# Kernel optimization log

Hardware: AMD Instinct MI355X
Metric: run time of the kernel (lower is better)

Reference implementation:

```python
import jax, jax.numpy as jnp
import numpy as np

N, E = 100000, 640000
H, EDGE_D, ATOM_D, RD, L = 128, 10, 25, 64, 4


def _gelu(t):
    return jax.nn.gelu(t, approximate=True)  # tanh approximation, matches torch GELU(approximate='tanh')


def _mlp2(t, w1, b1, w2, b2):
    return _gelu(t @ w1 + b1) @ w2 + b2


def setup_inputs() -> dict:
    key = jax.random.key(0)
    ks = iter(jax.random.split(key, 64))
    s = 0.05
    d = {}
    d['x'] = jax.random.normal(next(ks), (N, ATOM_D), jnp.float32)
    d['edge_index'] = jax.random.randint(next(ks), (2, E), 0, N, jnp.int32)
    d['edge_attr'] = jax.random.normal(next(ks), (E, EDGE_D), jnp.float32)
    d['enc_w1'] = jax.random.normal(next(ks), (ATOM_D, H)) * s
    d['enc_b1'] = jnp.zeros((H,))
    d['enc_w2'] = jax.random.normal(next(ks), (H, H)) * s
    d['enc_b2'] = jnp.zeros((H,))
    d['edge_w1'] = jax.random.normal(next(ks), (L, EDGE_D, H)) * s
    d['edge_b1'] = jnp.zeros((L, H))
    d['edge_w2'] = jax.random.normal(next(ks), (L, H, H)) * s
    d['edge_b2'] = jnp.zeros((L, H))
    d['msg_w1'] = jax.random.normal(next(ks), (L, H, H)) * s
    d['msg_b1'] = jnp.zeros((L, H))
    d['msg_w2'] = jax.random.normal(next(ks), (L, H, H)) * s
    d['msg_b2'] = jnp.zeros((L, H))
    d['gate_w'] = jax.random.normal(next(ks), (L, 2 * H, H)) * s
    d['gate_b'] = jnp.zeros((L, H))
    d['ln_g'] = jnp.ones((L, H))
    d['ln_b'] = jnp.zeros((L, H))
    for name in ('ion', 'pka', 'acid'):
        d[name + '_w1'] = jax.random.normal(next(ks), (H, RD)) * s
        d[name + '_b1'] = jnp.zeros((RD,))
        d[name + '_w2'] = jax.random.normal(next(ks), (RD, 1)) * s
        d[name + '_b2'] = jnp.zeros((1,))
    return d


def reference(x, edge_index, edge_attr, enc_w1, enc_b1, enc_w2, enc_b2,
              edge_w1, edge_b1, edge_w2, edge_b2,
              msg_w1, msg_b1, msg_w2, msg_b2,
              gate_w, gate_b, ln_g, ln_b,
              ion_w1, ion_b1, ion_w2, ion_b2,
              pka_w1, pka_b1, pka_w2, pka_b2,
              acid_w1, acid_b1, acid_w2, acid_b2):
    src, dst = edge_index[0], edge_index[1]
    n = x.shape[0]
    h = _mlp2(x, enc_w1, enc_b1, enc_w2, enc_b2)  # [N, H]
    ones_e = jnp.ones((src.shape[0],), x.dtype)
    count = jnp.clip(jax.ops.segment_sum(ones_e, dst, num_segments=n), 1.0)[:, None]  # [N,1]
    for i in range(L):
        ew = _mlp2(edge_attr, edge_w1[i], edge_b1[i], edge_w2[i], edge_b2[i])  # [E, H]
        msg = _mlp2(h[src], msg_w1[i], msg_b1[i], msg_w2[i], msg_b2[i]) * ew   # [E, H]
        agg = jax.ops.segment_sum(msg, dst, num_segments=n) / count           # [N, H] mean agg
        gate = jax.nn.sigmoid(jnp.concatenate([h, agg], axis=-1) @ gate_w[i] + gate_b[i])
        h = h + gate * agg
        mu = jnp.mean(h, axis=-1, keepdims=True)
        var = jnp.mean(jnp.square(h - mu), axis=-1, keepdims=True)
        h = (h - mu) * jax.lax.rsqrt(var + 1e-5) * ln_g[i] + ln_b[i]
    ion = _mlp2(h, ion_w1, ion_b1, ion_w2, ion_b2)
    pka = _mlp2(h, pka_w1, pka_b1, pka_w2, pka_b2)
    acid = _mlp2(h, acid_w1, acid_b1, acid_w2, acid_b2)
    return (ion, pka, acid)
```

## Files before the change

### kernel.cpp

```cpp
#include <hip/hip_runtime.h>
#include <math.h>

#define NN 100000
#define NN2 100032
#define NE 640000
#define H 128
#define AD 25
#define ED 10
#define RD 64
#define NL 4
#define NB_E (NE / 64 + 1)
#define NSB ((NN + 255) / 256)
#define CAP 256

typedef short bfrag __attribute__((ext_vector_type(8)));
typedef float floatx4 __attribute__((ext_vector_type(4)));
typedef unsigned short ushort;

#define MFMA(a, b, c) __builtin_amdgcn_mfma_f32_16x16x32_bf16(a, b, c, 0, 0, 0)

__device__ __forceinline__ ushort f2bf(float f) {
    unsigned u = __float_as_uint(f);
    unsigned r = (u + 0x7FFFu + ((u >> 16) & 1u)) >> 16;
    return (ushort)r;
}
__device__ __forceinline__ float bf2f(ushort b) {
    return __uint_as_float(((unsigned)b) << 16);
}
__device__ __forceinline__ float gelu_t(float x) {
    float u = 0.7978845608028654f * (x + 0.044715f * x * x * x);
    float e = __expf(2.0f * u);
    float th = 1.0f - 2.0f / (e + 1.0f);
    return 0.5f * x * (1.0f + th);
}
__device__ __forceinline__ float sigm(float x) {
    return 1.0f / (1.0f + __expf(-x));
}

__global__ void k_wtall(ushort* __restrict__ wt,
                        const float* __restrict__ s0, const float* __restrict__ s1,
                        const float* __restrict__ s2, const float* __restrict__ s3,
                        const float* __restrict__ s4, const float* __restrict__ s5,
                        const float* __restrict__ s6, const float* __restrict__ s7,
                        const float* __restrict__ s8, const float* __restrict__ s9) {
    int idx = blockIdx.x * 256 + threadIdx.x;
    const float* src;
    int Ks, N, Kd, off;
    if (idx < 4096)        { src = s0; Ks = 25;  N = 128; Kd = 32;  off = 0; }
    else if (idx < 20480)  { src = s1; Ks = 128; N = 128; Kd = 128; off = 4096; }
    else if (idx < 36864)  { src = s2; Ks = 10;  N = 128; Kd = 32;  off = 20480; }
    else if (idx < 102400) { src = s3; Ks = 128; N = 128; Kd = 128; off = 36864; }
    else if (idx < 167936) { src = s4; Ks = 128; N = 128; Kd = 128; off = 102400; }
    else if (idx < 233472) { src = s5; Ks = 128; N = 128; Kd = 128; off = 167936; }
    else if (idx < 364544) { src = s6; Ks = 256; N = 128; Kd = 256; off = 233472; }
    else if (idx < 372736) { src = s7; Ks = 128; N = 64;  Kd = 128; off = 364544; }
    else if (idx < 380928) { src = s8; Ks = 128; N = 64;  Kd = 128; off = 372736; }
    else if (idx < 389120) { src = s9; Ks = 128; N = 64;  Kd = 128; off = 380928; }
    else return;
    int lidx = idx - off;
    int nk = N * Kd;
    int b = lidx / nk;
    int rem = lidx - b * nk;
    int n = rem / Kd, k = rem - n * Kd;
    float v = (k < Ks) ? src[((size_t)b * Ks + k) * N + n] : 0.0f;
    wt[idx] = f2bf(v);
}

__global__ void k_cvt(const float* __restrict__ src, ushort* __restrict__ dst,
                      int rs, int Ks, int Kd, int total) {
    for (int idx = blockIdx.x * 256 + threadIdx.x; idx < total; idx += gridDim.x * 256) {
        int r = idx / Kd, k = idx - r * Kd;
        dst[idx] = (r < rs && k < Ks) ? f2bf(src[(size_t)r * Ks + k]) : 0;
    }
}
__global__ void k_cvtperm(const float* __restrict__ ea, const int* __restrict__ perm,
                          ushort* __restrict__ out) {
    int j = blockIdx.x * 256 + threadIdx.x;
    if (j >= NE) return;
    const float* src = ea + (size_t)perm[j] * ED;
    unsigned u[8];
#pragma unroll
    for (int k = 0; k < 5; ++k)
        u[k] = (unsigned)f2bf(src[2 * k]) | ((unsigned)f2bf(src[2 * k + 1]) << 16);
    u[5] = u[6] = u[7] = 0u;
    uint4* o = (uint4*)(out + (size_t)j * 16);
    uint4 a; a.x = u[0]; a.y = u[1]; a.z = u[2]; a.w = u[3];
    uint4 b; b.x = u[4]; b.y = u[5]; b.z = u[6]; b.w = u[7];
    o[0] = a; o[1] = b;
}

__global__ void k_hist(const int* __restrict__ ei, int* __restrict__ hist) {
    int e = blockIdx.x * 256 + threadIdx.x;
    if (e < NE) atomicAdd(&hist[ei[NE + e]], 1);
}
__global__ void k_scan1(const int* __restrict__ hist, int* __restrict__ incl,
                        int* __restrict__ bsum) {
    __shared__ int s[256];
    int tid = threadIdx.x;
    int i = blockIdx.x * 256 + tid;
    s[tid] = (i < NN) ? hist[i] : 0;
    __syncthreads();
    for (int off = 1; off < 256; off <<= 1) {
        int t = (tid >= off) ? s[tid - off] : 0;
        __syncthreads();
        s[tid] += t;
        __syncthreads();
    }
    if (i < NN) incl[i] = s[tid];
    if (tid == 255) bsum[blockIdx.x] = s[255];
}
__global__ void k_scan2(int* __restrict__ bsum) {
    __shared__ int s[512];
    int tid = threadIdx.x;
    s[tid] = (tid < NSB) ? bsum[tid] : 0;
    __syncthreads();
    for (int off = 1; off < 512; off <<= 1) {
        int t = (tid >= off) ? s[tid - off] : 0;
        __syncthreads();
        s[tid] += t;
        __syncthreads();
    }
    if (tid < NSB) bsum[tid] = (tid > 0) ? s[tid - 1] : 0;
}
__global__ void k_scan3(const int* __restrict__ hist, const int* __restrict__ incl,
                        const int* __restrict__ bsum, int* __restrict__ row_ptr) {
    int i = blockIdx.x * 256 + threadIdx.x;
    if (i < NN) row_ptr[i] = bsum[blockIdx.x] + incl[i] - hist[i];
    if (i == 0) row_ptr[NN] = NE;
}
__global__ void k_scatter(const int* __restrict__ ei, int* __restrict__ cursor,
                          int* __restrict__ perm) {
    int e = blockIdx.x * 256 + threadIdx.x;
    if (e < NE) {
        int d = ei[NE + e];
        int pos = atomicAdd(&cursor[d], 1);
        perm[pos] = e;
    }
}
__global__ void k_blockrange(const int* __restrict__ row_ptr, int* __restrict__ nf,
                             int* __restrict__ nl) {
    int n = blockIdx.x * 256 + threadIdx.x;
    if (n < NN) {
        int b = row_ptr[n] >> 6;
        atomicMin(&nf[b], n);
        atomicMax(&nl[b], n);
    }
}

template <int K1>
__global__ void __launch_bounds__(256)
k_mlp2mf(const ushort* __restrict__ Abf, ushort* __restrict__ Obf,
         const ushort* __restrict__ W1t, const float* __restrict__ B1,
         const ushort* __restrict__ W2t, const float* __restrict__ B2) {
    __shared__ ushort sH[64 * 136];
    const int tid = threadIdx.x;
    const int w = tid >> 6, lane = tid & 63, lr = lane & 15, lg = lane >> 4;
    const int rowB = blockIdx.x * 64 + w * 16 + lr;

    bfrag bvv[K1 / 32];
#pragma unroll
    for (int kb = 0; kb < K1 / 32; ++kb)
        bvv[kb] = *(const bfrag*)(Abf + (size_t)rowB * K1 + kb * 32 + lg * 8);

    floatx4 acc[8];
#pragma unroll
    for (int t = 0; t < 8; ++t) acc[t] = (floatx4){0.f, 0.f, 0.f, 0.f};
#pragma unroll
    for (int kb = 0; kb < K1 / 32; ++kb) {
#pragma unroll
        for (int t = 0; t < 8; ++t) {
            bfrag av = *(const bfrag*)(W1t + (t * 16 + lr) * K1 + kb * 32 + lg * 8);
            acc[t] = MFMA(av, bvv[kb], acc[t]);
        }
    }
    ushort* sHrow = sH + (w * 16 + lr) * 136;
#pragma unroll
    for (int t = 0; t < 8; ++t) {
        const float4 b1 = *(const float4*)(B1 + t * 16 + lg * 4);
        float h0 = gelu_t(acc[t][0] + b1.x), h1 = gelu_t(acc[t][1] + b1.y);
        float h2 = gelu_t(acc[t][2] + b1.z), h3 = gelu_t(acc[t][3] + b1.w);
        uint2 p;
        p.x = (unsigned)f2bf(h0) | ((unsigned)f2bf(h1) << 16);
        p.y = (unsigned)f2bf(h2) | ((unsigned)f2bf(h3) << 16);
        *(uint2*)(sHrow + t * 16 + lg * 4) = p;
    }
#pragma unroll
    for (int t = 0; t < 8; ++t) acc[t] = (floatx4){0.f, 0.f, 0.f, 0.f};
#pragma unroll
    for (int kb = 0; kb < 4; ++kb) {
        bfrag av = *(const bfrag*)(sH + (w * 16 + lr) * 136 + kb * 32 + lg * 8);
#pragma unroll
        for (int t = 0; t < 8; ++t) {
            bfrag bv = *(const bfrag*)(W2t + (t * 16 + lr) * 128 + kb * 32 + lg * 8);
            acc[t] = MFMA(av, bv, acc[t]);
        }
    }
    const int rowD = blockIdx.x * 64 + w * 16 + lg * 4;
#pragma unroll
    for (int t = 0; t < 8; ++t) {
        const int col = t * 16 + lr;
        const float b2 = B2[col];
#pragma unroll
        for (int r = 0; r < 4; ++r) {
            int row = rowD + r;
            if (row < NN) Obf[(size_t)row * 128 + col] = f2bf(acc[t][r] + b2);
        }
    }
}

__global__ void __launch_bounds__(256)
k_ew(const ushort* __restrict__ eap, ushort* __restrict__ ewp, int S,
     const ushort* __restrict__ W1t, const float* __restrict__ B1,
     const ushort* __restrict__ W2t, const float* __restrict__ B2) {
    __shared__ ushort sea[128 * 40];
    __shared__ ushort sH[4][16 * 136];
    const int tid = threadIdx.x;
    const int w = tid >> 6, lane = tid & 63, lr = lane & 15, lg = lane >> 4;
    const int jl0 = blockIdx.x * 128;

    {
        int r = tid >> 1, half = tid & 1;
        int j = S + jl0 + r;
        uint4 z; z.x = z.y = z.z = z.w = 0u;
        uint4 v = z;
        if (j < NE) v = *(const uint4*)(eap + (size_t)j * 16 + half * 8);
        *(uint4*)(sea + r * 40 + half * 8) = v;
        *(uint4*)(sea + r * 40 + 16 + half * 8) = z;
    }
    bfrag av1[8];
#pragma unroll
    for (int t = 0; t < 8; ++t)
        av1[t] = *(const bfrag*)(W1t + (t * 16 + lr) * 32 + lg * 8);
    __syncthreads();

    for (int rt = 0; rt < 2; ++rt) {
        const int row_l = w * 32 + rt * 16;
        floatx4 acc[8];
#pragma unroll
        for (int t = 0; t < 8; ++t) acc[t] = (floatx4){0.f, 0.f, 0.f, 0.f};
        bfrag bv = *(const bfrag*)(sea + (row_l + lr) * 40 + lg * 8);
#pragma unroll
        for (int t = 0; t < 8; ++t) acc[t] = MFMA(av1[t], bv, acc[t]);
        ushort* sHr = sH[w] + lr * 136;
#pragma unroll
        for (int t = 0; t < 8; ++t) {
            const float4 b1 = *(const float4*)(B1 + t * 16 + lg * 4);
            float h0 = gelu_t(acc[t][0] + b1.x), h1 = gelu_t(acc[t][1] + b1.y);
            float h2 = gelu_t(acc[t][2] + b1.z), h3 = gelu_t(acc[t][3] + b1.w);
            uint2 p;
            p.x = (unsigned)f2bf(h0) | ((unsigned)f2bf(h1) << 16);
            p.y = (unsigned)f2bf(h2) | ((unsigned)f2bf(h3) << 16);
            *(uint2*)(sHr + t * 16 + lg * 4) = p;
        }
#pragma unroll
        for (int t = 0; t < 8; ++t) acc[t] = (floatx4){0.f, 0.f, 0.f, 0.f};
#pragma unroll
        for (int kb = 0; kb < 4; ++kb) {
            bfrag av = *(const bfrag*)(sH[w] + lr * 136 + kb * 32 + lg * 8);
#pragma unroll
            for (int t = 0; t < 8; ++t) {
                bfrag bw = *(const bfrag*)(W2t + (t * 16 + lr) * 128 + kb * 32 + lg * 8);
                acc[t] = MFMA(bw, av, acc[t]);
            }
        }
        const int jl = jl0 + row_l + lr;
        if (S + jl < NE) {
            ushort* orow = ewp + (size_t)jl * 128;
#pragma unroll
            for (int t = 0; t < 8; ++t) {
                const float4 b2 = *(const float4*)(B2 + t * 16 + lg * 4);
                uint2 p;
                p.x = (unsigned)f2bf(acc[t][0] + b2.x) |
                      ((unsigned)f2bf(acc[t][1] + b2.y) << 16);
                p.y = (unsigned)f2bf(acc[t][2] + b2.z) |
                      ((unsigned)f2bf(acc[t][3] + b2.w) << 16);
                *(uint2*)(orow + t * 16 + lg * 4) = p;
            }
        }
    }
}

__global__ void __launch_bounds__(256)
k_gms(const int* __restrict__ ei, const int* __restrict__ perm,
      const int* __restrict__ row_ptr, const int* __restrict__ nf,
      const int* __restrict__ nl, const ushort* __restrict__ ewp, int S,
      const ushort* __restrict__ mbf, ushort* __restrict__ aggbf) {
    __shared__ int ssrc[CAP], sdst[CAP], sseg[CAP];
    __shared__ int snode[64];
    __shared__ float sinvd[64];
    __shared__ float sagg[64 * 132];
    __shared__ int swtot[4];
    __shared__ int s_nseg;

    const int b = blockIdx.x;
    const int n0 = nf[b];
    if (n0 >= NN) return;
    const int n1 = nl[b];
    const int e0 = row_ptr[n0];
    int ne = row_ptr[n1 + 1] - e0;
    if (ne <= 0) return;
    const int ncl = (ne < CAP) ? ne : CAP;

    const int tid = threadIdx.x;
    const int w = tid >> 6, lane = tid & 63;

    for (int i = tid; i < 64 * 132; i += 256) sagg[i] = 0.0f;

    int dstv = -1 - tid;
    if (tid < ncl) {
        int e = perm[e0 + tid];
        ssrc[tid] = ei[e];
        dstv = ei[NE + e];
    }
    sdst[tid] = dstv;
    __syncthreads();

    int f = 0;
    if (tid < ncl) f = (tid == 0) ? 1 : (sdst[tid] != sdst[tid - 1]);
    unsigned long long mk = __ballot(f);
    int incl = __popcll(mk & (~0ull >> (63 - lane)));
    if (lane == 63) swtot[w] = incl;
    __syncthreads();
    int woff = 0;
    for (int i = 0; i < w; ++i) woff += swtot[i];
    int segid = woff + incl;
    sseg[tid] = segid - 1;
    if (f) {
        int s = segid - 1;
        snode[s] = dstv;
        sinvd[s] = 1.0f / (float)(row_ptr[dstv + 1] - row_ptr[dstv]);
    }
    if (tid == 255) s_nseg = segid;
    __syncthreads();
    const int nseg = s_nseg;

    const int c0 = (tid & 31) * 4;
    const int g = tid >> 5;
    const int chunk = (ncl + 7) >> 3;
    const int j0 = g * chunk;
    const int j1 = (j0 + chunk < ncl) ? (j0 + chunk) : ncl;
    const int be = e0 - S;
    int cs = -1;
    float v0 = 0.f, v1 = 0.f, v2 = 0.f, v3 = 0.f;
    uint2 ewc, mvc;
    if (j0 < j1) {
        ewc = *(const uint2*)(ewp + (size_t)(be + j0) * 128 + c0);
        mvc = *(const uint2*)(mbf + (size_t)ssrc[j0] * 128 + c0);
    }
    for (int j = j0; j < j1; ++j) {
        uint2 ewn = ewc, mvn = mvc;
        if (j + 1 < j1) {
            ewn = *(const uint2*)(ewp + (size_t)(be + j + 1) * 128 + c0);
            mvn = *(const uint2*)(mbf + (size_t)ssrc[j + 1] * 128 + c0);
        }
        float a0 = bf2f((ushort)(ewc.x & 0xFFFF)) * bf2f((ushort)(mvc.x & 0xFFFF));
        float a1 = bf2f((ushort)(ewc.x >> 16)) * bf2f((ushort)(mvc.x >> 16));
        float a2 = bf2f((ushort)(ewc.y & 0xFFFF)) * bf2f((ushort)(mvc.y & 0xFFFF));
        float a3 = bf2f((ushort)(ewc.y >> 16)) * bf2f((ushort)(mvc.y >> 16));
        int sg = sseg[j];
        if (sg != cs) {
            if (cs >= 0) {
                float* p = &sagg[cs * 132 + c0];
                atomicAdd(p + 0, v0); atomicAdd(p + 1, v1);
                atomicAdd(p + 2, v2); atomicAdd(p + 3, v3);
            }
            cs = sg; v0 = a0; v1 = a1; v2 = a2; v3 = a3;
        } else {
            v0 += a0; v1 += a1; v2 += a2; v3 += a3;
        }
        ewc = ewn; mvc = mvn;
    }
    if (cs >= 0) {
        float* p = &sagg[cs * 132 + c0];
        atomicAdd(p + 0, v0); atomicAdd(p + 1, v1);
        atomicAdd(p + 2, v2); atomicAdd(p + 3, v3);
    }
    __syncthreads();
    for (int i = tid; i < nseg * 32; i += 256) {
        int s = i >> 5, qd = i & 31;
        float inv = sinvd[s];
        const float* p = &sagg[s * 132 + qd * 4];
        uint2 pk;
        pk.x = (unsigned)f2bf(p[0] * inv) | ((unsigned)f2bf(p[1] * inv) << 16);
        pk.y = (unsigned)f2bf(p[2] * inv) | ((unsigned)f2bf(p[3] * inv) << 16);
        *(uint2*)(aggbf + (size_t)snode[s] * 128 + qd * 4) = pk;
    }
}

template <int WITH_MSG>
__global__ void __launch_bounds__(256)
k_gatemlp(ushort* __restrict__ hbf, const ushort* __restrict__ aggbf,
          const ushort* __restrict__ GWt, const float* __restrict__ GB,
          const float* __restrict__ LNG, const float* __restrict__ LNB,
          const ushort* __restrict__ W1t, const float* __restrict__ B1,
          const ushort* __restrict__ W2t, const float* __restrict__ B2,
          ushort* __restrict__ mbf) {
    __shared__ ushort sA[64 * 136];
    const int tid = threadIdx.x;
    const int w = tid >> 6, lane = tid & 63, lr = lane & 15, lg = lane >> 4;
    const int row = blockIdx.x * 64 + w * 16 + lr;

    bfrag bvv[8];
    uint2 hp[8], ap[8];
#pragma unroll
    for (int kb = 0; kb < 4; ++kb)
        bvv[kb] = *(const bfrag*)(hbf + (size_t)row * 128 + kb * 32 + lg * 8);
#pragma unroll
    for (int kb = 0; kb < 4; ++kb)
        bvv[4 + kb] = *(const bfrag*)(aggbf + (size_t)row * 128 + kb * 32 + lg * 8);
#pragma unroll
    for (int t = 0; t < 8; ++t) {
        hp[t] = *(const uint2*)(hbf + (size_t)row * 128 + t * 16 + lg * 4);
        ap[t] = *(const uint2*)(aggbf + (size_t)row * 128 + t * 16 + lg * 4);
    }

    floatx4 acc[8];
#pragma unroll
    for (int t = 0; t < 8; ++t) acc[t] = (floatx4){0.f, 0.f, 0.f, 0.f};
#pragma unroll
    for (int kb = 0; kb < 8; ++kb) {
#pragma unroll
        for (int t = 0; t < 8; ++t) {
            bfrag av = *(const bfrag*)(GWt + (t * 16 + lr) * 256 + kb * 32 + lg * 8);
            acc[t] = MFMA(av, bvv[kb], acc[t]);
        }
    }
    float o[8][4];
    float s = 0.0f;
#pragma unroll
    for (int t = 0; t < 8; ++t) {
        const int c0 = t * 16 + lg * 4;
        const float4 gb = *(const float4*)(GB + c0);
        float h0 = bf2f((ushort)(hp[t].x & 0xFFFF)), h1 = bf2f((ushort)(hp[t].x >> 16));
        float h2 = bf2f((ushort)(hp[t].y & 0xFFFF)), h3 = bf2f((ushort)(hp[t].y >> 16));
        float a0 = bf2f((ushort)(ap[t].x & 0xFFFF)), a1 = bf2f((ushort)(ap[t].x >> 16));
        float a2 = bf2f((ushort)(ap[t].y & 0xFFFF)), a3 = bf2f((ushort)(ap[t].y >> 16));
        o[t][0] = h0 + sigm(acc[t][0] + gb.x) * a0;
        o[t][1] = h1 + sigm(acc[t][1] + gb.y) * a1;
        o[t][2] = h2 + sigm(acc[t][2] + gb.z) * a2;
        o[t][3] = h3 + sigm(acc[t][3] + gb.w) * a3;
        s += o[t][0] + o[t][1] + o[t][2] + o[t][3];
    }
    s += __shfl_xor(s, 16);
    s += __shfl_xor(s, 32);
    const float mu = s * (1.0f / 128.0f);
    float q = 0.0f;
#pragma unroll
    for (int t = 0; t < 8; ++t)
#pragma unroll
        for (int r = 0; r < 4; ++r) {
            float dx = o[t][r] - mu;
            q = fmaf(dx, dx, q);
        }
    q += __shfl_xor(q, 16);
    q += __shfl_xor(q, 32);
    const float rs = rsqrtf(q * (1.0f / 128.0f) + 1e-5f);

    ushort* sArow = sA + (w * 16 + lr) * 136;
#pragma unroll
    for (int t = 0; t < 8; ++t) {
        const int c0 = t * 16 + lg * 4;
        const float4 g4 = *(const float4*)(LNG + c0);
        const float4 b4 = *(const float4*)(LNB + c0);
        float r0 = fmaf((o[t][0] - mu) * rs, g4.x, b4.x);
        float r1 = fmaf((o[t][1] - mu) * rs, g4.y, b4.y);
        float r2 = fmaf((o[t][2] - mu) * rs, g4.z, b4.z);
        float r3 = fmaf((o[t][3] - mu) * rs, g4.w, b4.w);
        uint2 pk;
        pk.x = (unsigned)f2bf(r0) | ((unsigned)f2bf(r1) << 16);
        pk.y = (unsigned)f2bf(r2) | ((unsigned)f2bf(r3) << 16);
        if (row < NN) *(uint2*)(hbf + (size_t)row * 128 + c0) = pk;
        if (WITH_MSG) *(uint2*)(sArow + c0) = pk;
    }

    if (WITH_MSG) {
#pragma unroll
        for (int t = 0; t < 8; ++t) acc[t] = (floatx4){0.f, 0.f, 0.f, 0.f};
#pragma unroll
        for (int kb = 0; kb < 4; ++kb) {
            bfrag bv = *(const bfrag*)(sA + (w * 16 + lr) * 136 + kb * 32 + lg * 8);
#pragma unroll
            for (int t = 0; t < 8; ++t) {
                bfrag av = *(const bfrag*)(W1t + (t * 16 + lr) * 128 + kb * 32 + lg * 8);
                acc[t] = MFMA(av, bv, acc[t]);
            }
        }
#pragma unroll
        for (int t = 0; t < 8; ++t) {
            const float4 b1 = *(const float4*)(B1 + t * 16 + lg * 4);
            float h0 = gelu_t(acc[t][0] + b1.x), h1 = gelu_t(acc[t][1] + b1.y);
            float h2 = gelu_t(acc[t][2] + b1.z), h3 = gelu_t(acc[t][3] + b1.w);
            uint2 p;
            p.x = (unsigned)f2bf(h0) | ((unsigned)f2bf(h1) << 16);
            p.y = (unsigned)f2bf(h2) | ((unsigned)f2bf(h3) << 16);
            *(uint2*)(sArow + t * 16 + lg * 4) = p;
        }
#pragma unroll
        for (int t = 0; t < 8; ++t) acc[t] = (floatx4){0.f, 0.f, 0.f, 0.f};
#pragma unroll
        for (int kb = 0; kb < 4; ++kb) {
            bfrag av = *(const bfrag*)(sA + (w * 16 + lr) * 136 + kb * 32 + lg * 8);
#pragma unroll
            for (int t = 0; t < 8; ++t) {
                bfrag bv = *(const bfrag*)(W2t + (t * 16 + lr) * 128 + kb * 32 + lg * 8);
                acc[t] = MFMA(av, bv, acc[t]);
            }
        }
        const int rowD = blockIdx.x * 64 + w * 16 + lg * 4;
#pragma unroll
        for (int t = 0; t < 8; ++t) {
            const int col = t * 16 + lr;
            const float b2 = B2[col];
#pragma unroll
            for (int r = 0; r < 4; ++r) {
                int rw = rowD + r;
                if (rw < NN) mbf[(size_t)rw * 128 + col] = f2bf(acc[t][r] + b2);
            }
        }
    }
}

__global__ void __launch_bounds__(256)
k_headsmf(const ushort* __restrict__ hbf, float* __restrict__ OUT,
          const ushort* __restrict__ WHt,
          const float* __restrict__ b1a, const float* __restrict__ b1b, const float* __restrict__ b1c,
          const float* __restrict__ w2a, const float* __restrict__ w2b, const float* __restrict__ w2c,
          const float* __restrict__ b2a, const float* __restrict__ b2b, const float* __restrict__ b2c) {
    const int tid = threadIdx.x;
    const int w = tid >> 6, lane = tid & 63, lr = lane & 15, lg = lane >> 4;
    const int row = blockIdx.x * 64 + w * 16 + lr;

    floatx4 acc[12];
#pragma unroll
    for (int t = 0; t < 12; ++t) acc[t] = (floatx4){0.f, 0.f, 0.f, 0.f};
    bfrag bvv[4];
#pragma unroll
    for (int kb = 0; kb < 4; ++kb)
        bvv[kb] = *(const bfrag*)(hbf + (size_t)row * 128 + kb * 32 + lg * 8);
#pragma unroll
    for (int kb = 0; kb < 4; ++kb) {
#pragma unroll
        for (int t = 0; t < 12; ++t) {
            bfrag av = *(const bfrag*)(WHt + (t * 16 + lr) * 128 + kb * 32 + lg * 8);
            acc[t] = MFMA(av, bvv[kb], acc[t]);
        }
    }
    const float* b1s[3] = {b1a, b1b, b1c};
    const float* w2s[3] = {w2a, w2b, w2c};
    float p[3] = {0.f, 0.f, 0.f};
#pragma unroll
    for (int t = 0; t < 12; ++t) {
        const int head = t >> 2;
        const int c0 = (t & 3) * 16 + lg * 4;
        const float4 b1 = *(const float4*)(b1s[head] + c0);
        const float4 w2 = *(const float4*)(w2s[head] + c0);
        p[head] += gelu_t(acc[t][0] + b1.x) * w2.x;
        p[head] += gelu_t(acc[t][1] + b1.y) * w2.y;
        p[head] += gelu_t(acc[t][2] + b1.z) * w2.z;
        p[head] += gelu_t(acc[t][3] + b1.w) * w2.w;
    }
#pragma unroll
    for (int hd = 0; hd < 3; ++hd) {
        p[hd] += __shfl_xor(p[hd], 16);
        p[hd] += __shfl_xor(p[hd], 32);
    }
    if (lg == 0 && row < NN) {
        OUT[0 * NN + row] = p[0] + b2a[0];
        OUT[1 * NN + row] = p[1] + b2b[0];
        OUT[2 * NN + row] = p[2] + b2c[0];
    }
}

extern "C" void kernel_launch(void* const* d_in, const int* in_sizes, int n_in,
                              void* d_out, int out_size, void* d_ws, size_t ws_size,
                              hipStream_t stream) {
    const float* x       = (const float*)d_in[0];
    const int*   ei      = (const int*)d_in[1];
    const float* ea      = (const float*)d_in[2];
    const float* enc_w1  = (const float*)d_in[3];
    const float* enc_b1  = (const float*)d_in[4];
    const float* enc_w2  = (const float*)d_in[5];
    const float* enc_b2  = (const float*)d_in[6];
    const float* edge_w1 = (const float*)d_in[7];
    const float* edge_b1 = (const float*)d_in[8];
    const float* edge_w2 = (const float*)d_in[9];
    const float* edge_b2 = (const float*)d_in[10];
    const float* msg_w1  = (const float*)d_in[11];
    const float* msg_b1  = (const float*)d_in[12];
    const float* msg_w2  = (const float*)d_in[13];
    const float* msg_b2  = (const float*)d_in[14];
    const float* gate_w  = (const float*)d_in[15];
    const float* gate_b  = (const float*)d_in[16];
    const float* ln_g    = (const float*)d_in[17];
    const float* ln_b    = (const float*)d_in[18];
    const float* hw[12];
    for (int t = 0; t < 12; ++t) hw[t] = (const float*)d_in[19 + t];

    const size_t NNH = (size_t)NN2 * H;
    ushort* hbf   = (ushort*)d_ws;
    ushort* mbf   = hbf + NNH;
    ushort* aggbf = mbf + NNH;
    ushort* xbf   = aggbf + NNH;
    ushort* eapbf = xbf + (size_t)NN2 * 32;
    ushort* wt    = eapbf + (size_t)NE * 16;
    ushort* wt_enc1 = wt;
    ushort* wt_enc2 = wt_enc1 + 128 * 32;
    ushort* wt_e1   = wt_enc2 + 128 * 128;
    ushort* wt_e2   = wt_e1 + 4 * 128 * 32;
    ushort* wt_m1   = wt_e2 + 4 * 128 * 128;
    ushort* wt_m2   = wt_m1 + 4 * 128 * 128;
    ushort* wt_g    = wt_m2 + 4 * 128 * 128;
    ushort* wt_h    = wt_g + 4 * 128 * 256;
    int* row_ptr = (int*)(wt_h + 192 * 128 + 64);
    int* perm    = row_ptr + 100352;
    int* nf      = perm + NE;
    int* nl      = nf + 10240;
    int* hist    = nl + 10240;
    int* incl    = hist + 100352;
    int* cursor  = incl + 100352;
    int* bsum    = cursor + 100352;
    uintptr_t ewp_addr = ((uintptr_t)(bsum + 512) + 15) & ~(uintptr_t)15;
    ushort* ewp = (ushort*)ewp_addr;
    const size_t used = ewp_addr - (uintptr_t)d_ws;

    int P = 4;
    size_t rows = NE / 4 + 1024;
    if (ws_size >= used + (size_t)NE * 128 * 2) { P = 1; rows = NE; }
    else if (ws_size >= used + ((size_t)NE / 2 + 1024) * 128 * 2) { P = 2; rows = NE / 2 + 1024; }
    const int PE = NE / P;
    const int NGB = 10000 / P;
    const int ewblk = (int)(rows / 128);

    hipMemsetAsync(hist, 0, NN * sizeof(int), stream);
    hipMemsetAsync(nf, 0x7f, NB_E * sizeof(int), stream);
    hipMemsetAsync(nl, 0xff, NB_E * sizeof(int), stream);
    hipMemsetAsync(aggbf, 0, NNH * sizeof(ushort), stream);
    k_hist<<<(NE + 255) / 256, 256, 0, stream>>>(ei, hist);
    k_scan1<<<NSB, 256, 0, stream>>>(hist, incl, bsum);
    k_scan2<<<1, 512, 0, stream>>>(bsum);
    k_scan3<<<NSB, 256, 0, stream>>>(hist, incl, bsum, row_ptr);
    hipMemcpyAsync(cursor, row_ptr, NN * sizeof(int), hipMemcpyDeviceToDevice, stream);
    k_scatter<<<(NE + 255) / 256, 256, 0, stream>>>(ei, cursor, perm);
    k_blockrange<<<(NN + 255) / 256, 256, 0, stream>>>(row_ptr, nf, nl);

    k_wtall<<<1520, 256, 0, stream>>>(wt, enc_w1, enc_w2, edge_w1, edge_w2,
                                      msg_w1, msg_w2, gate_w, hw[0], hw[4], hw[8]);
    k_cvt<<<3200, 256, 0, stream>>>(x, xbf, NN, 25, 32, NN2 * 32);
    k_cvtperm<<<(NE + 255) / 256, 256, 0, stream>>>(ea, perm, eapbf);

    const int ntiles = NN2 / 64;
    k_mlp2mf<32><<<ntiles, 256, 0, stream>>>(xbf, hbf,
        wt_enc1, enc_b1, wt_enc2, enc_b2);
    k_mlp2mf<128><<<ntiles, 256, 0, stream>>>(hbf, mbf,
        wt_m1, msg_b1, wt_m2, msg_b2);

    for (int l = 0; l < NL; ++l) {
        for (int p = 0; p < P; ++p) {
            const int S = p * PE;
            k_ew<<<ewblk, 256, 0, stream>>>(eapbf, ewp, S,
                wt_e1 + (size_t)l * 128 * 32, edge_b1 + l * H,
                wt_e2 + (size_t)l * 128 * 128, edge_b2 + l * H);
            const int nb = (p == P - 1) ? (NGB + 1) : NGB;
            k_gms<<<nb, 256, 0, stream>>>(ei, perm, row_ptr,
                nf + p * NGB, nl + p * NGB, ewp, S, mbf, aggbf);
        }
        if (l < NL - 1) {
            k_gatemlp<1><<<ntiles, 256, 0, stream>>>(hbf, aggbf,
                wt_g + (size_t)l * 128 * 256, gate_b + l * H,
                ln_g + l * H, ln_b + l * H,
                wt_m1 + (size_t)(l + 1) * 128 * 128, msg_b1 + (l + 1) * H,
                wt_m2 + (size_t)(l + 1) * 128 * 128, msg_b2 + (l + 1) * H, mbf);
        } else {
            k_gatemlp<0><<<ntiles, 256, 0, stream>>>(hbf, aggbf,
                wt_g + (size_t)l * 128 * 256, gate_b + l * H,
                ln_g + l * H, ln_b + l * H,
                nullptr, nullptr, nullptr, nullptr, nullptr);
        }
    }

    k_headsmf<<<ntiles, 256, 0, stream>>>(hbf, (float*)d_out, wt_h,
        hw[1], hw[5], hw[9], hw[2], hw[6], hw[10], hw[3], hw[7], hw[11]);
}
```

Baseline: 2.230 ms.

## Fuse gate, layernorm and next message MLP into the gather-scatter aggregation kernel

The per-node gate, residual, layernorm and next-layer message MLP now run inside the aggregation kernel, reading the aggregated sums straight from shared memory. This removes the bf16 aggregate buffer round-trip, its memset and the separate full-node gate kernel. Nodes with no incoming edges are collected into a list and handled by a small extra kernel. Messages are double-buffered so the next layer's messages can be written while other blocks still read the current ones. The edge-feature prefetch in the gather loop is dropped. The cost is a heavier aggregation kernel with more registers and MFMA work per block, plus scattered row writes.

```diff
diff --git a/kernel.cpp b/kernel.cpp
--- a/kernel.cpp
+++ b/kernel.cpp
@@ -138,12 +138,17 @@
     }
 }
 __global__ void k_blockrange(const int* __restrict__ row_ptr, int* __restrict__ nf,
-                             int* __restrict__ nl) {
+                             int* __restrict__ nl, int* __restrict__ d0l,
+                             int* __restrict__ d0c) {
     int n = blockIdx.x * 256 + threadIdx.x;
     if (n < NN) {
         int b = row_ptr[n] >> 6;
         atomicMin(&nf[b], n);
         atomicMax(&nl[b], n);
+        if (row_ptr[n + 1] == row_ptr[n]) {
+            int p = atomicAdd(d0c, 1);
+            d0l[p] = n;
+        }
     }
 }
 
@@ -280,11 +285,17 @@
     }
 }
 
+template <int WITH_MSG>
 __global__ void __launch_bounds__(256)
-k_gms(const int* __restrict__ ei, const int* __restrict__ perm,
-      const int* __restrict__ row_ptr, const int* __restrict__ nf,
-      const int* __restrict__ nl, const ushort* __restrict__ ewp, int S,
-      const ushort* __restrict__ mbf, ushort* __restrict__ aggbf) {
+k_gmsfull(const int* __restrict__ ei, const int* __restrict__ perm,
+          const int* __restrict__ row_ptr, const int* __restrict__ nf,
+          const int* __restrict__ nl, const ushort* __restrict__ ewp, int S,
+          const ushort* __restrict__ mcur, ushort* __restrict__ hbf,
+          ushort* __restrict__ mnext,
+          const ushort* __restrict__ GWt, const float* __restrict__ GB,
+          const float* __restrict__ LNG, const float* __restrict__ LNB,
+          const ushort* __restrict__ W1t, const float* __restrict__ B1,
+          const ushort* __restrict__ W2t, const float* __restrict__ B2) {
     __shared__ int ssrc[CAP], sdst[CAP], sseg[CAP];
     __shared__ int snode[64];
     __shared__ float sinvd[64];
@@ -305,6 +316,7 @@
     const int w = tid >> 6, lane = tid & 63;
 
     for (int i = tid; i < 64 * 132; i += 256) sagg[i] = 0.0f;
+    if (tid < 64) sinvd[tid] = 0.0f;
 
     int dstv = -1 - tid;
     if (tid < ncl) {
@@ -334,116 +346,86 @@
     __syncthreads();
     const int nseg = s_nseg;
 
-    const int c0 = (tid & 31) * 4;
-    const int g = tid >> 5;
-    const int chunk = (ncl + 7) >> 3;
-    const int j0 = g * chunk;
-    const int j1 = (j0 + chunk < ncl) ? (j0 + chunk) : ncl;
-    const int be = e0 - S;
-    int cs = -1;
-    float v0 = 0.f, v1 = 0.f, v2 = 0.f, v3 = 0.f;
-    uint2 ewc, mvc;
-    if (j0 < j1) {
-        ewc = *(const uint2*)(ewp + (size_t)(be + j0) * 128 + c0);
-        mvc = *(const uint2*)(mbf + (size_t)ssrc[j0] * 128 + c0);
-    }
-    for (int j = j0; j < j1; ++j) {
-        uint2 ewn = ewc, mvn = mvc;
-        if (j + 1 < j1) {
-            ewn = *(const uint2*)(ewp + (size_t)(be + j + 1) * 128 + c0);
-            mvn = *(const uint2*)(mbf + (size_t)ssrc[j + 1] * 128 + c0);
-        }
-        float a0 = bf2f((ushort)(ewc.x & 0xFFFF)) * bf2f((ushort)(mvc.x & 0xFFFF));
-        float a1 = bf2f((ushort)(ewc.x >> 16)) * bf2f((ushort)(mvc.x >> 16));
-        float a2 = bf2f((ushort)(ewc.y & 0xFFFF)) * bf2f((ushort)(mvc.y & 0xFFFF));
-        float a3 = bf2f((ushort)(ewc.y >> 16)) * bf2f((ushort)(mvc.y >> 16));
-        int sg = sseg[j];
-        if (sg != cs) {
-            if (cs >= 0) {
-                float* p = &sagg[cs * 132 + c0];
-                atomicAdd(p + 0, v0); atomicAdd(p + 1, v1);
-                atomicAdd(p + 2, v2); atomicAdd(p + 3, v3);
-            }
-            cs = sg; v0 = a0; v1 = a1; v2 = a2; v3 = a3;
+    {
+        const int c0 = (tid & 31) * 4;
+        const int g = tid >> 5;
+        const int chunk = (ncl + 7) >> 3;
+        const int j0 = g * chunk;
+        const int j1 = (j0 + chunk < ncl) ? (j0 + chunk) : ncl;
+        const int be = e0 - S;
+        int cs = -1;
+        float v0 = 0.f, v1 = 0.f, v2 = 0.f, v3 = 0.f;
+        for (int j = j0; j < j1; ++j) {
+            uint2 ew = *(const uint2*)(ewp + (size_t)(be + j) * 128 + c0);
+            uint2 mv = *(const uint2*)(mcur + (size_t)ssrc[j] * 128 + c0);
+            float a0 = bf2f((ushort)(ew.x & 0xFFFF)) * bf2f((ushort)(mv.x & 0xFFFF));
+            float a1 = bf2f((ushort)(ew.x >> 16)) * bf2f((ushort)(mv.x >> 16));
+            float a2 = bf2f((ushort)(ew.y & 0xFFFF)) * bf2f((ushort)(mv.y & 0xFFFF));
+            float a3 = bf2f((ushort)(ew.y >> 16)) * bf2f((ushort)(mv.y >> 16));
+            int sg = sseg[j];
+            if (sg != cs) {
+                if (cs >= 0) {
+                    float* p = &sagg[cs * 132 + c0];
+                    atomicAdd(p + 0, v0); atomicAdd(p + 1, v1);
+                    atomicAdd(p + 2, v2); atomicAdd(p + 3, v3);
+                }
+                cs = sg; v0 = a0; v1 = a1; v2 = a2; v3 = a3;
+            } else {
+                v0 += a0; v1 += a1; v2 += a2; v3 += a3;
+            }
+        }
+        if (cs >= 0) {
+            float* p = &sagg[cs * 132 + c0];
+            atomicAdd(p + 0, v0); atomicAdd(p + 1, v1);
+            atomicAdd(p + 2, v2); atomicAdd(p + 3, v3);
+        }
+    }
+    __syncthreads();
+
+    const int lr = lane & 15, lg = lane >> 4;
+    const int sIdx = w * 16 + lr;
+    const int node = (sIdx < nseg) ? snode[sIdx] : 0;
+    const float inv = sinvd[sIdx];
+
+    floatx4 acc[8];
+#pragma unroll
+    for (int t = 0; t < 8; ++t) acc[t] = (floatx4){0.f, 0.f, 0.f, 0.f};
+#pragma unroll
+    for (int kb = 0; kb < 8; ++kb) {
+        bfrag bv;
+        if (kb < 4) {
+            bv = *(const bfrag*)(hbf + (size_t)node * 128 + kb * 32 + lg * 8);
         } else {
-            v0 += a0; v1 += a1; v2 += a2; v3 += a3;
-        }
-        ewc = ewn; mvc = mvn;
-    }
-    if (cs >= 0) {
-        float* p = &sagg[cs * 132 + c0];
-        atomicAdd(p + 0, v0); atomicAdd(p + 1, v1);
-        atomicAdd(p + 2, v2); atomicAdd(p + 3, v3);
-    }
-    __syncthreads();
-    for (int i = tid; i < nseg * 32; i += 256) {
-        int s = i >> 5, qd = i & 31;
-        float inv = sinvd[s];
-        const float* p = &sagg[s * 132 + qd * 4];
-        uint2 pk;
-        pk.x = (unsigned)f2bf(p[0] * inv) | ((unsigned)f2bf(p[1] * inv) << 16);
-        pk.y = (unsigned)f2bf(p[2] * inv) | ((unsigned)f2bf(p[3] * inv) << 16);
-        *(uint2*)(aggbf + (size_t)snode[s] * 128 + qd * 4) = pk;
-    }
-}
-
-template <int WITH_MSG>
-__global__ void __launch_bounds__(256)
-k_gatemlp(ushort* __restrict__ hbf, const ushort* __restrict__ aggbf,
-          const ushort* __restrict__ GWt, const float* __restrict__ GB,
-          const float* __restrict__ LNG, const float* __restrict__ LNB,
-          const ushort* __restrict__ W1t, const float* __restrict__ B1,
-          const ushort* __restrict__ W2t, const float* __restrict__ B2,
-          ushort* __restrict__ mbf) {
-    __shared__ ushort sA[64 * 136];
-    const int tid = threadIdx.x;
-    const int w = tid >> 6, lane = tid & 63, lr = lane & 15, lg = lane >> 4;
-    const int row = blockIdx.x * 64 + w * 16 + lr;
-
-    bfrag bvv[8];
-    uint2 hp[8], ap[8];
-#pragma unroll
-    for (int kb = 0; kb < 4; ++kb)
-        bvv[kb] = *(const bfrag*)(hbf + (size_t)row * 128 + kb * 32 + lg * 8);
-#pragma unroll
-    for (int kb = 0; kb < 4; ++kb)
-        bvv[4 + kb] = *(const bfrag*)(aggbf + (size_t)row * 128 + kb * 32 + lg * 8);
-#pragma unroll
-    for (int t = 0; t < 8; ++t) {
-        hp[t] = *(const uint2*)(hbf + (size_t)row * 128 + t * 16 + lg * 4);
-        ap[t] = *(const uint2*)(aggbf + (size_t)row * 128 + t * 16 + lg * 4);
-    }
-
-    floatx4 acc[8];
-#pragma unroll
-    for (int t = 0; t < 8; ++t) acc[t] = (floatx4){0.f, 0.f, 0.f, 0.f};
-#pragma unroll
-    for (int kb = 0; kb < 8; ++kb) {
+            const float* ar = &sagg[sIdx * 132 + (kb - 4) * 32 + lg * 8];
+#pragma unroll
+            for (int i = 0; i < 8; ++i) ((ushort*)&bv)[i] = f2bf(ar[i] * inv);
+        }
 #pragma unroll
         for (int t = 0; t < 8; ++t) {
             bfrag av = *(const bfrag*)(GWt + (t * 16 + lr) * 256 + kb * 32 + lg * 8);
-            acc[t] = MFMA(av, bvv[kb], acc[t]);
+            acc[t] = MFMA(av, bv, acc[t]);
         }
     }
     float o[8][4];
-    float s = 0.0f;
+    float ssum = 0.0f;
 #pragma unroll
     for (int t = 0; t < 8; ++t) {
         const int c0 = t * 16 + lg * 4;
         const float4 gb = *(const float4*)(GB + c0);
-        float h0 = bf2f((ushort)(hp[t].x & 0xFFFF)), h1 = bf2f((ushort)(hp[t].x >> 16));
-        float h2 = bf2f((ushort)(hp[t].y & 0xFFFF)), h3 = bf2f((ushort)(hp[t].y >> 16));
-        float a0 = bf2f((ushort)(ap[t].x & 0xFFFF)), a1 = bf2f((ushort)(ap[t].x >> 16));
-        float a2 = bf2f((ushort)(ap[t].y & 0xFFFF)), a3 = bf2f((ushort)(ap[t].y >> 16));
+        uint2 hp = *(const uint2*)(hbf + (size_t)node * 128 + c0);
+        const float* ar = &sagg[sIdx * 132 + c0];
+        float a0 = ar[0] * inv, a1 = ar[1] * inv, a2 = ar[2] * inv, a3 = ar[3] * inv;
+        float h0 = bf2f((ushort)(hp.x & 0xFFFF)), h1 = bf2f((ushort)(hp.x >> 16));
+        float h2 = bf2f((ushort)(hp.y & 0xFFFF)), h3 = bf2f((ushort)(hp.y >> 16));
         o[t][0] = h0 + sigm(acc[t][0] + gb.x) * a0;
         o[t][1] = h1 + sigm(acc[t][1] + gb.y) * a1;
         o[t][2] = h2 + sigm(acc[t][2] + gb.z) * a2;
         o[t][3] = h3 + sigm(acc[t][3] + gb.w) * a3;
-        s += o[t][0] + o[t][1] + o[t][2] + o[t][3];
-    }
-    s += __shfl_xor(s, 16);
-    s += __shfl_xor(s, 32);
-    const float mu = s * (1.0f / 128.0f);
+        ssum += o[t][0] + o[t][1] + o[t][2] + o[t][3];
+    }
+    ssum += __shfl_xor(ssum, 16);
+    ssum += __shfl_xor(ssum, 32);
+    const float mu = ssum * (1.0f / 128.0f);
     float q = 0.0f;
 #pragma unroll
     for (int t = 0; t < 8; ++t)
@@ -456,7 +438,8 @@
     q += __shfl_xor(q, 32);
     const float rs = rsqrtf(q * (1.0f / 128.0f) + 1e-5f);
 
-    ushort* sArow = sA + (w * 16 + lr) * 136;
+    ushort* sAbase = (ushort*)&sagg[(size_t)w * 16 * 132];
+    ushort* sArow = sAbase + lr * 136;
 #pragma unroll
     for (int t = 0; t < 8; ++t) {
         const int c0 = t * 16 + lg * 4;
@@ -469,7 +452,7 @@
         uint2 pk;
         pk.x = (unsigned)f2bf(r0) | ((unsigned)f2bf(r1) << 16);
         pk.y = (unsigned)f2bf(r2) | ((unsigned)f2bf(r3) << 16);
-        if (row < NN) *(uint2*)(hbf + (size_t)row * 128 + c0) = pk;
+        if (sIdx < nseg) *(uint2*)(hbf + (size_t)node * 128 + c0) = pk;
         if (WITH_MSG) *(uint2*)(sArow + c0) = pk;
     }
 
@@ -478,7 +461,7 @@
         for (int t = 0; t < 8; ++t) acc[t] = (floatx4){0.f, 0.f, 0.f, 0.f};
 #pragma unroll
         for (int kb = 0; kb < 4; ++kb) {
-            bfrag bv = *(const bfrag*)(sA + (w * 16 + lr) * 136 + kb * 32 + lg * 8);
+            bfrag bv = *(const bfrag*)(sAbase + lr * 136 + kb * 32 + lg * 8);
 #pragma unroll
             for (int t = 0; t < 8; ++t) {
                 bfrag av = *(const bfrag*)(W1t + (t * 16 + lr) * 128 + kb * 32 + lg * 8);
@@ -499,22 +482,131 @@
         for (int t = 0; t < 8; ++t) acc[t] = (floatx4){0.f, 0.f, 0.f, 0.f};
 #pragma unroll
         for (int kb = 0; kb < 4; ++kb) {
-            bfrag av = *(const bfrag*)(sA + (w * 16 + lr) * 136 + kb * 32 + lg * 8);
+            bfrag av = *(const bfrag*)(sAbase + lr * 136 + kb * 32 + lg * 8);
 #pragma unroll
             for (int t = 0; t < 8; ++t) {
                 bfrag bv = *(const bfrag*)(W2t + (t * 16 + lr) * 128 + kb * 32 + lg * 8);
                 acc[t] = MFMA(av, bv, acc[t]);
             }
         }
-        const int rowD = blockIdx.x * 64 + w * 16 + lg * 4;
+        int on[4];
+#pragma unroll
+        for (int r = 0; r < 4; ++r) {
+            int so = w * 16 + lg * 4 + r;
+            on[r] = (so < nseg) ? snode[so] : -1;
+        }
 #pragma unroll
         for (int t = 0; t < 8; ++t) {
             const int col = t * 16 + lr;
             const float b2 = B2[col];
 #pragma unroll
+            for (int r = 0; r < 4; ++r)
+                if (on[r] >= 0) mnext[(size_t)on[r] * 128 + col] = f2bf(acc[t][r] + b2);
+        }
+    }
+}
+
+template <int WITH_MSG>
+__global__ void __launch_bounds__(256)
+k_deg0(const int* __restrict__ lst, const int* __restrict__ cnt,
+       ushort* __restrict__ hbf, ushort* __restrict__ mnext,
+       const float* __restrict__ LNG, const float* __restrict__ LNB,
+       const ushort* __restrict__ W1t, const float* __restrict__ B1,
+       const ushort* __restrict__ W2t, const float* __restrict__ B2) {
+    __shared__ ushort sA[4][16 * 136];
+    const int tid = threadIdx.x;
+    const int w = tid >> 6, lane = tid & 63, lr = lane & 15, lg = lane >> 4;
+    const int total = cnt[0];
+
+    for (int base = blockIdx.x * 64; base < total; base += gridDim.x * 64) {
+        const int idx = base + w * 16 + lr;
+        const int node = (idx < total) ? lst[idx] : 0;
+        float o[8][4];
+        float ssum = 0.0f;
+#pragma unroll
+        for (int t = 0; t < 8; ++t) {
+            const int c0 = t * 16 + lg * 4;
+            uint2 hp = *(const uint2*)(hbf + (size_t)node * 128 + c0);
+            o[t][0] = bf2f((ushort)(hp.x & 0xFFFF));
+            o[t][1] = bf2f((ushort)(hp.x >> 16));
+            o[t][2] = bf2f((ushort)(hp.y & 0xFFFF));
+            o[t][3] = bf2f((ushort)(hp.y >> 16));
+            ssum += o[t][0] + o[t][1] + o[t][2] + o[t][3];
+        }
+        ssum += __shfl_xor(ssum, 16);
+        ssum += __shfl_xor(ssum, 32);
+        const float mu = ssum * (1.0f / 128.0f);
+        float q = 0.0f;
+#pragma unroll
+        for (int t = 0; t < 8; ++t)
+#pragma unroll
             for (int r = 0; r < 4; ++r) {
-                int rw = rowD + r;
-                if (rw < NN) mbf[(size_t)rw * 128 + col] = f2bf(acc[t][r] + b2);
+                float dx = o[t][r] - mu;
+                q = fmaf(dx, dx, q);
+            }
+        q += __shfl_xor(q, 16);
+        q += __shfl_xor(q, 32);
+        const float rs = rsqrtf(q * (1.0f / 128.0f) + 1e-5f);
+
+        ushort* sArow = sA[w] + lr * 136;
+#pragma unroll
+        for (int t = 0; t < 8; ++t) {
+            const int c0 = t * 16 + lg * 4;
+            const float4 g4 = *(const float4*)(LNG + c0);
+            const float4 b4 = *(const float4*)(LNB + c0);
+            float r0 = fmaf((o[t][0] - mu) * rs, g4.x, b4.x);
+            float r1 = fmaf((o[t][1] - mu) * rs, g4.y, b4.y);
+            float r2 = fmaf((o[t][2] - mu) * rs, g4.z, b4.z);
+            float r3 = fmaf((o[t][3] - mu) * rs, g4.w, b4.w);
+            uint2 pk;
+            pk.x = (unsigned)f2bf(r0) | ((unsigned)f2bf(r1) << 16);
+            pk.y = (unsigned)f2bf(r2) | ((unsigned)f2bf(r3) << 16);
+            if (idx < total) *(uint2*)(hbf + (size_t)node * 128 + c0) = pk;
+            if (WITH_MSG) *(uint2*)(sArow + c0) = pk;
+        }
+        if (WITH_MSG) {
+            floatx4 acc[8];
+#pragma unroll
+            for (int t = 0; t < 8; ++t) acc[t] = (floatx4){0.f, 0.f, 0.f, 0.f};
+#pragma unroll
+            for (int kb = 0; kb < 4; ++kb) {
+                bfrag bv = *(const bfrag*)(sA[w] + lr * 136 + kb * 32 + lg * 8);
+#pragma unroll
+                for (int t = 0; t < 8; ++t) {
+                    bfrag av = *(const bfrag*)(W1t + (t * 16 + lr) * 128 + kb * 32 + lg * 8);
+                    acc[t] = MFMA(av, bv, acc[t]);
+                }
+            }
+#pragma unroll
+            for (int t = 0; t < 8; ++t) {
+                const float4 b1 = *(const float4*)(B1 + t * 16 + lg * 4);
+                float h0 = gelu_t(acc[t][0] + b1.x), h1 = gelu_t(acc[t][1] + b1.y);
+                float h2 = gelu_t(acc[t][2] + b1.z), h3 = gelu_t(acc[t][3] + b1.w);
+                uint2 p;
+                p.x = (unsigned)f2bf(h0) | ((unsigned)f2bf(h1) << 16);
+                p.y = (unsigned)f2bf(h2) | ((unsigned)f2bf(h3) << 16);
+                *(uint2*)(sArow + t * 16 + lg * 4) = p;
+            }
+#pragma unroll
+            for (int t = 0; t < 8; ++t) acc[t] = (floatx4){0.f, 0.f, 0.f, 0.f};
+#pragma unroll
+            for (int kb = 0; kb < 4; ++kb) {
+                bfrag av = *(const bfrag*)(sA[w] + lr * 136 + kb * 32 + lg * 8);
+#pragma unroll
+                for (int t = 0; t < 8; ++t) {
+                    bfrag bv = *(const bfrag*)(W2t + (t * 16 + lr) * 128 + kb * 32 + lg * 8);
+                    acc[t] = MFMA(av, bv, acc[t]);
+                }
+            }
+#pragma unroll
+            for (int t = 0; t < 8; ++t) {
+                const int col = t * 16 + lr;
+                const float b2 = B2[col];
+#pragma unroll
+                for (int r = 0; r < 4; ++r) {
+                    int i2 = base + w * 16 + lg * 4 + r;
+                    if (i2 < total) mnext[(size_t)lst[i2] * 128 + col] = f2bf(acc[t][r] + b2);
+                }
             }
         }
     }
@@ -598,9 +690,9 @@
 
     const size_t NNH = (size_t)NN2 * H;
     ushort* hbf   = (ushort*)d_ws;
-    ushort* mbf   = hbf + NNH;
-    ushort* aggbf = mbf + NNH;
-    ushort* xbf   = aggbf + NNH;
+    ushort* mbf0  = hbf + NNH;
+    ushort* mbf1  = mbf0 + NNH;
+    ushort* xbf   = mbf1 + NNH;
     ushort* eapbf = xbf + (size_t)NN2 * 32;
     ushort* wt    = eapbf + (size_t)NE * 16;
     ushort* wt_enc1 = wt;
@@ -619,6 +711,8 @@
     int* incl    = hist + 100352;
     int* cursor  = incl + 100352;
     int* bsum    = cursor + 100352;
+    int* d0l     = hist;
+    int* d0c     = bsum + 500;
     uintptr_t ewp_addr = ((uintptr_t)(bsum + 512) + 15) & ~(uintptr_t)15;
     ushort* ewp = (ushort*)ewp_addr;
     const size_t used = ewp_addr - (uintptr_t)d_ws;
@@ -634,14 +728,14 @@
     hipMemsetAsync(hist, 0, NN * sizeof(int), stream);
     hipMemsetAsync(nf, 0x7f, NB_E * sizeof(int), stream);
     hipMemsetAsync(nl, 0xff, NB_E * sizeof(int), stream);
-    hipMemsetAsync(aggbf, 0, NNH * sizeof(ushort), stream);
     k_hist<<<(NE + 255) / 256, 256, 0, stream>>>(ei, hist);
     k_scan1<<<NSB, 256, 0, stream>>>(hist, incl, bsum);
     k_scan2<<<1, 512, 0, stream>>>(bsum);
     k_scan3<<<NSB, 256, 0, stream>>>(hist, incl, bsum, row_ptr);
     hipMemcpyAsync(cursor, row_ptr, NN * sizeof(int), hipMemcpyDeviceToDevice, stream);
     k_scatter<<<(NE + 255) / 256, 256, 0, stream>>>(ei, cursor, perm);
-    k_blockrange<<<(NN + 255) / 256, 256, 0, stream>>>(row_ptr, nf, nl);
+    hipMemsetAsync(d0c, 0, sizeof(int), stream);
+    k_blockrange<<<(NN + 255) / 256, 256, 0, stream>>>(row_ptr, nf, nl, d0l, d0c);
 
     k_wtall<<<1520, 256, 0, stream>>>(wt, enc_w1, enc_w2, edge_w1, edge_w2,
                                       msg_w1, msg_w2, gate_w, hw[0], hw[4], hw[8]);
@@ -651,31 +745,42 @@
     const int ntiles = NN2 / 64;
     k_mlp2mf<32><<<ntiles, 256, 0, stream>>>(xbf, hbf,
         wt_enc1, enc_b1, wt_enc2, enc_b2);
-    k_mlp2mf<128><<<ntiles, 256, 0, stream>>>(hbf, mbf,
+    k_mlp2mf<128><<<ntiles, 256, 0, stream>>>(hbf, mbf0,
         wt_m1, msg_b1, wt_m2, msg_b2);
 
+    const ushort* mc = mbf0;
+    ushort* mn = mbf1;
     for (int l = 0; l < NL; ++l) {
+        const ushort* gwl = wt_g + (size_t)l * 128 * 256;
+        const float* gbl = gate_b + l * H;
+        const float* lngl = ln_g + l * H;
+        const float* lnbl = ln_b + l * H;
+        const ushort* mw1 = wt_m1 + (size_t)(l + 1) * 128 * 128;
+        const float* mb1 = msg_b1 + (l + 1) * H;
+        const ushort* mw2 = wt_m2 + (size_t)(l + 1) * 128 * 128;
+        const float* mb2 = msg_b2 + (l + 1) * H;
         for (int p = 0; p < P; ++p) {
             const int S = p * PE;
             k_ew<<<ewblk, 256, 0, stream>>>(eapbf, ewp, S,
                 wt_e1 + (size_t)l * 128 * 32, edge_b1 + l * H,
                 wt_e2 + (size_t)l * 128 * 128, edge_b2 + l * H);
             const int nb = (p == P - 1) ? (NGB + 1) : NGB;
-            k_gms<<<nb, 256, 0, stream>>>(ei, perm, row_ptr,
-                nf + p * NGB, nl + p * NGB, ewp, S, mbf, aggbf);
-        }
-        if (l < NL - 1) {
-            k_gatemlp<1><<<ntiles, 256, 0, stream>>>(hbf, aggbf,
-                wt_g + (size_t)l * 128 * 256, gate_b + l * H,
-                ln_g + l * H, ln_b + l * H,
-                wt_m1 + (size_t)(l + 1) * 128 * 128, msg_b1 + (l + 1) * H,
-                wt_m2 + (size_t)(l + 1) * 128 * 128, msg_b2 + (l + 1) * H, mbf);
-        } else {
-            k_gatemlp<0><<<ntiles, 256, 0, stream>>>(hbf, aggbf,
-                wt_g + (size_t)l * 128 * 256, gate_b + l * H,
-                ln_g + l * H, ln_b + l * H,
-                nullptr, nullptr, nullptr, nullptr, nullptr);
-        }
+            if (l < NL - 1)
+                k_gmsfull<1><<<nb, 256, 0, stream>>>(ei, perm, row_ptr,
+                    nf + p * NGB, nl + p * NGB, ewp, S, mc, hbf, mn,
+                    gwl, gbl, lngl, lnbl, mw1, mb1, mw2, mb2);
+            else
+                k_gmsfull<0><<<nb, 256, 0, stream>>>(ei, perm, row_ptr,
+                    nf + p * NGB, nl + p * NGB, ewp, S, mc, hbf, mn,
+                    gwl, gbl, lngl, lnbl, nullptr, nullptr, nullptr, nullptr);
+        }
+        if (l < NL - 1)
+            k_deg0<1><<<64, 256, 0, stream>>>(d0l, d0c, hbf, mn,
+                lngl, lnbl, mw1, mb1, mw2, mb2);
+        else
+            k_deg0<0><<<64, 256, 0, stream>>>(d0l, d0c, hbf, mn,
+                lngl, lnbl, nullptr, nullptr, nullptr, nullptr);
+        const ushort* tmp = mc; mc = mn; mn = (ushort*)tmp;
     }
 
     k_headsmf<<<ntiles, 256, 0, stream>>>(hbf, (float*)d_out, wt_h,
```

Result: slower. 3.825 ms (+71.5%).
